# Optimization experiments

Hardware: AMD Instinct MI355X
Metric: run time of the kernel (lower is better)

Reference implementation:

```python
import jax, jax.numpy as jnp
import numpy as np
from jax.scipy.special import logsumexp

SINKHORN_ALPHA = 20.0
OT_MAX_ITER = 100
STOP_THR = 0.005


def setup_inputs() -> dict:
    key = jax.random.key(0)
    k1, k2 = jax.random.split(key)
    x = jax.random.normal(k1, (256, 384), dtype=jnp.float32)   # topic embeddings [K, D]
    y = jax.random.normal(k2, (32768, 384), dtype=jnp.float32)  # word embeddings  [V, D]
    return {"x": x, "y": y}


def reference(x, y):
    n, m = x.shape[0], y.shape[0]
    # FASTopic pairwise_euclidean_distance: squared euclidean cost [n, m]
    M = jnp.sum(x * x, axis=1, keepdims=True) + jnp.sum(y * y, axis=1) - 2.0 * (x @ y.T)
    a = jnp.full((n, 1), 1.0 / n, dtype=M.dtype)
    b = jnp.full((m, 1), 1.0 / m, dtype=M.dtype)
    log_a = jnp.log(a + 1e-30)
    log_b = jnp.log(b + 1e-30)
    log_K0 = -M * SINKHORN_ALPHA

    # State trick: the original mutates log_K only at the periodic absorption step
    # (log_K += log_u + log_v.T). We keep log_K = log_K0 + cum_u + cum_v.T so the
    # carried state is only O(n + m) vectors; math is identical.
    def body(state):
        log_u, log_v, cum_u, cum_v, err, cpt = state
        log_K = log_K0 + cum_u + cum_v.T                                    # [n, m]
        log_v_n = log_b - logsumexp(log_K.T + log_u.T, axis=1)[:, None]     # [m, 1]
        log_u_n = log_a - logsumexp(log_K + log_v_n.T, axis=1)[:, None]     # [n, 1]
        cpt_n = cpt + 1

        def absorb(_):
            cu = cum_u + log_u_n
            cv = cum_v + log_v_n
            lK = log_K0 + cu + cv.T
            # marginal check with log_u = log_v = 0 (matches check_convergence)
            row = jnp.exp(logsumexp(lK, axis=1))[:, None]
            col = jnp.exp(logsumexp(lK, axis=0))[:, None]
            e = jnp.maximum(jnp.max(jnp.abs(row - a)), jnp.max(jnp.abs(col - b)))
            return jnp.zeros_like(log_u_n), jnp.zeros_like(log_v_n), cu, cv, e

        def keep(_):
            return log_u_n, log_v_n, cum_u, cum_v, err

        lu, lv, cu, cv, e = jax.lax.cond(cpt_n % 50 == 1, absorb, keep, None)
        return (lu, lv, cu, cv, e, cpt_n)

    def cond_fn(state):
        err, cpt = state[4], state[5]
        return (err > STOP_THR) & (cpt < OT_MAX_ITER)

    init = (jnp.zeros((n, 1), M.dtype), jnp.zeros((m, 1), M.dtype),
            jnp.zeros((n, 1), M.dtype), jnp.zeros((m, 1), M.dtype),
            jnp.array(1.0, M.dtype), jnp.array(0, jnp.int32))
    log_u, log_v, cum_u, cum_v, _, _ = jax.lax.while_loop(cond_fn, body, init)

    log_K = log_K0 + cum_u + cum_v.T
    transp = jnp.exp(log_u) * (jnp.exp(log_K) * jnp.exp(log_v).T)  # diag(u) K diag(v)
    loss_ETP = jnp.sum(transp * M)
    return loss_ETP, transp
```

## Files before the change

kernel.cpp:

```cpp
#include <hip/hip_runtime.h>
#include <math.h>


#define N_TOPIC 256
#define N_WORD  32768

static constexpr float LOG_A = -5.545177444479562f;
static constexpr float LOG_B = -10.397207708399179f;
static constexpr float BVAL  = 3.0517578125e-05f;

typedef float f32x4 __attribute__((ext_vector_type(4)));
typedef short bf16x8 __attribute__((ext_vector_type(8)));

#define PIN4(v) asm volatile("" : "+v"((v).x), "+v"((v).y), "+v"((v).z), "+v"((v).w))

__global__ __launch_bounds__(256) void init_k(
    const float* __restrict__ x, const float* __restrict__ y,
    float* __restrict__ nx, float* __restrict__ ny, float* __restrict__ su,
    unsigned* __restrict__ colerr, int* __restrict__ active,
    int* __restrict__ counters, float* __restrict__ out)
{
    const int b = blockIdx.x, t = threadIdx.x;
    const int w = t >> 6, l = t & 63;
    if (b < 8192) {
        const int r = (b << 2) + w;
        const float4* y4 = (const float4*)y;
        float4 v = y4[r * 96 + l];
        float s = v.x * v.x + v.y * v.y + v.z * v.z + v.w * v.w;
        if (l < 32) {
            float4 u = y4[r * 96 + 64 + l];
            s += u.x * u.x + u.y * u.y + u.z * u.z + u.w * u.w;
        }
        for (int off = 32; off; off >>= 1) s += __shfl_down(s, off);
        if (l == 0) ny[r] = s;
    } else if (b < 8256) {
        const int r = ((b - 8192) << 2) + w;
        const float4* x4 = (const float4*)x;
        float4 v = x4[r * 96 + l];
        float s = v.x * v.x + v.y * v.y + v.z * v.z + v.w * v.w;
        if (l < 32) {
            float4 u = x4[r * 96 + 64 + l];
            s += u.x * u.x + u.y * u.y + u.z * u.z + u.w * u.w;
        }
        for (int off = 32; off; off >>= 1) s += __shfl_down(s, off);
        if (l == 0) { nx[r] = s; su[r] = -20.f * s; }
    } else {
        for (int k = t; k < 4096; k += 256) counters[k] = 0;
        if (t == 0) { colerr[0] = 0u; colerr[1] = 0u; active[0] = 1; out[0] = 0.f; }
    }
}

static __device__ __forceinline__ void split3(float v, ushort& h0, ushort& h1, ushort& h2)
{
    unsigned u0 = __float_as_uint(v);
    h0 = (ushort)(u0 >> 16);
    float r1 = v - __uint_as_float(u0 & 0xFFFF0000u);
    unsigned u1 = __float_as_uint(r1);
    h1 = (ushort)(u1 >> 16);
    float r2 = r1 - __uint_as_float(u1 & 0xFFFF0000u);
    h2 = (ushort)(__float_as_uint(r2) >> 16);
}

static __device__ __forceinline__ bool bar_arrive(int* cnt, int ph, int t, int* lastf)
{
    __threadfence();
    if (t == 0) *lastf = (atomicAdd(&cnt[ph], 1) == 255);
    __syncthreads();
    return *lastf != 0;
}
static __device__ __forceinline__ void bar_release(int* gen, int ph, int t)
{
    __threadfence();
    if (t == 0) atomicExch(gen, ph);
}
static __device__ __forceinline__ void bar_wait(int* gen, int ph, int t)
{
    if (t == 0) {
        while (atomicCAS(gen, -1, -1) < ph) __builtin_amdgcn_s_sleep(2);
    }
    __syncthreads();
    __threadfence();
}

__global__ __launch_bounds__(256, 1) void fused_k(
    const float* __restrict__ x, const float* __restrict__ y,
    float* __restrict__ G,
    float* __restrict__ su, const float* __restrict__ nx,
    const float* __restrict__ ny, float2* __restrict__ pms,
    float* __restrict__ prow, int* __restrict__ cnt, int* __restrict__ gen,
    unsigned* __restrict__ colerr, int* __restrict__ active,
    float* __restrict__ out)
{
    __shared__ __align__(16) char smem[63488];
    __shared__ int lastf;
    float4* xs4 = (float4*)smem;
    ushort* ys0 = (ushort*)(smem + 32768);
    ushort* ys1 = (ushort*)(smem + 43008);
    ushort* ys2 = (ushort*)(smem + 53248);
    float* su_lds = (float*)smem;
    float* mm    = (float*)(smem + 1024);
    float* ss    = (float*)(smem + 5120);
    float* Mcol  = (float*)(smem + 9216);
    float* Wlds  = (float*)(smem + 9728);
    float* ecol  = (float*)(smem + 10240);
    float* Rlds  = (float*)(smem + 10752);
    float* errb  = (float*)(smem + 11776);
    float* nxl   = (float*)(smem + 12288);
    float* nyl   = (float*)(smem + 13312);
    float* pq    = (float*)(smem + 13824);

    const int t   = threadIdx.x;
    const int b   = blockIdx.x;
    const int w   = t >> 6, ln = t & 63, q = ln >> 4, l15 = ln & 15;
    const int jq  = t & 31, ig = t >> 5;
    const int c0  = jq << 2;
    const int jy0 = b << 7;
    int ph = 1;

    const float4* x4 = (const float4*)x;
    const float4* y4 = (const float4*)y;

    {
        f32x4 acc[4][8];
#pragma unroll
        for (int mi = 0; mi < 4; ++mi)
#pragma unroll
            for (int nj = 0; nj < 8; ++nj) acc[mi][nj] = (f32x4){0.f, 0.f, 0.f, 0.f};

        for (int kc = 0; kc < 12; ++kc) {
            __syncthreads();
#pragma unroll
            for (int p = 0; p < 8; ++p) {
                const int f = (p << 8) + t;
                const int r = f >> 3, c4 = f & 7;
                xs4[(r << 3) + (c4 ^ (r & 7))] = x4[r * 96 + (kc << 3) + c4];
            }
#pragma unroll
            for (int p = 0; p < 4; ++p) {
                const int f = (p << 8) + t;
                const int r = f >> 3, c4 = f & 7;
                float4 vy = y4[(size_t)(jy0 + r) * 96 + (kc << 3) + c4];
                ushort a0,a1,a2,b0,b1,b2,g0,g1,g2,d0,d1,d2;
                split3(vy.x, a0,a1,a2); split3(vy.y, b0,b1,b2);
                split3(vy.z, g0,g1,g2); split3(vy.w, d0,d1,d2);
                *(ushort4*)&ys0[r * 40 + (c4 << 2)] = make_ushort4(a0,b0,g0,d0);
                *(ushort4*)&ys1[r * 40 + (c4 << 2)] = make_ushort4(a1,b1,g1,d1);
                *(ushort4*)&ys2[r * 40 + (c4 << 2)] = make_ushort4(a2,b2,g2,d2);
            }
            __syncthreads();

            union U8 { ushort u[8]; bf16x8 v; };
            bf16x8 A0[4], A1[4], A2[4];
#pragma unroll
            for (int mi = 0; mi < 4; ++mi) {
                const int row = (w << 6) + (mi << 4) + l15;
                const int base = row << 3;
                float4 xa = xs4[base + (((q << 1) + 0) ^ (row & 7))];
                float4 xb = xs4[base + (((q << 1) + 1) ^ (row & 7))];
                U8 u0, u1, u2;
                split3(xa.x, u0.u[0], u1.u[0], u2.u[0]);
                split3(xa.y, u0.u[1], u1.u[1], u2.u[1]);
                split3(xa.z, u0.u[2], u1.u[2], u2.u[2]);
                split3(xa.w, u0.u[3], u1.u[3], u2.u[3]);
                split3(xb.x, u0.u[4], u1.u[4], u2.u[4]);
                split3(xb.y, u0.u[5], u1.u[5], u2.u[5]);
                split3(xb.z, u0.u[6], u1.u[6], u2.u[6]);
                split3(xb.w, u0.u[7], u1.u[7], u2.u[7]);
                A0[mi] = u0.v; A1[mi] = u1.v; A2[mi] = u2.v;
            }
#pragma unroll
            for (int nj = 0; nj < 8; ++nj) {
                const int off = ((nj << 4) + l15) * 40 + (q << 3);
                bf16x8 B0 = *(const bf16x8*)&ys0[off];
                bf16x8 B1 = *(const bf16x8*)&ys1[off];
                bf16x8 B2 = *(const bf16x8*)&ys2[off];
#pragma unroll
                for (int mi = 0; mi < 4; ++mi) {
                    f32x4 c = acc[mi][nj];
                    c = __builtin_amdgcn_mfma_f32_16x16x32_bf16(A0[mi], B0, c, 0, 0, 0);
                    c = __builtin_amdgcn_mfma_f32_16x16x32_bf16(A0[mi], B1, c, 0, 0, 0);
                    c = __builtin_amdgcn_mfma_f32_16x16x32_bf16(A1[mi], B0, c, 0, 0, 0);
                    c = __builtin_amdgcn_mfma_f32_16x16x32_bf16(A1[mi], B1, c, 0, 0, 0);
                    c = __builtin_amdgcn_mfma_f32_16x16x32_bf16(A0[mi], B2, c, 0, 0, 0);
                    c = __builtin_amdgcn_mfma_f32_16x16x32_bf16(A2[mi], B0, c, 0, 0, 0);
                    acc[mi][nj] = c;
                }
            }
        }

#pragma unroll
        for (int mi = 0; mi < 4; ++mi) {
#pragma unroll
            for (int r = 0; r < 4; ++r) {
                const int R = (w << 6) + (mi << 4) + (q << 2) + r;
                float* grow = G + ((size_t)b << 15) + (size_t)R * 128;
#pragma unroll
                for (int nj = 0; nj < 8; ++nj)
                    grow[(nj << 4) + l15] = 40.f * acc[mi][nj][r];
            }
        }
    }

    __syncthreads();

    const float4* G4 = (const float4*)G;
    float4 tile[32];
#pragma unroll
    for (int k = 0; k < 32; ++k) {
        const int i = ig + (k << 3);
        tile[k] = G4[((size_t)b << 13) + (i << 5) + jq];
    }
#pragma unroll
    for (int k = 0; k < 32; ++k) PIN4(tile[k]);

    su_lds[t] = su[t];
    __syncthreads();

    {
        float m0=-INFINITY,m1=-INFINITY,m2=-INFINITY,m3=-INFINITY;
#pragma unroll
        for (int k = 0; k < 32; ++k) {
            const float sk = su_lds[ig + (k << 3)];
            m0=fmaxf(m0,tile[k].x+sk); m1=fmaxf(m1,tile[k].y+sk);
            m2=fmaxf(m2,tile[k].z+sk); m3=fmaxf(m3,tile[k].w+sk);
        }
        float s0=0.f,s1=0.f,s2=0.f,s3=0.f;
#pragma unroll
        for (int k = 0; k < 32; ++k) {
            const float sk = su_lds[ig + (k << 3)];
            s0+=__expf(tile[k].x+sk-m0); s1+=__expf(tile[k].y+sk-m1);
            s2+=__expf(tile[k].z+sk-m2); s3+=__expf(tile[k].w+sk-m3);
        }
        mm[ig*128+c0+0]=m0; ss[ig*128+c0+0]=s0;
        mm[ig*128+c0+1]=m1; ss[ig*128+c0+1]=s1;
        mm[ig*128+c0+2]=m2; ss[ig*128+c0+2]=s2;
        mm[ig*128+c0+3]=m3; ss[ig*128+c0+3]=s3;
        __syncthreads();
        if (t < 128) {
            float m=-INFINITY, s=0.f;
#pragma unroll
            for (int g = 0; g < 8; ++g) {
                float pmv=mm[g*128+t], psv=ss[g*128+t];
                float nm=fmaxf(m,pmv);
                s = s*__expf(m-nm) + psv*__expf(pmv-nm);
                m = nm;
            }
            Wlds[t] = LOG_B - (m + __logf(s));
        }
        __syncthreads();
    }
    {
#pragma unroll
        for (int k = 0; k < 32; ++k) {
            const int i = ig + (k << 3);
            float a0=tile[k].x+Wlds[c0], a1=tile[k].y+Wlds[c0+1];
            float a2=tile[k].z+Wlds[c0+2], a3=tile[k].w+Wlds[c0+3];
            pq[i*33+jq] = fmaxf(fmaxf(a0,a1), fmaxf(a2,a3));
        }
        __syncthreads();
        {
            float R=-INFINITY;
#pragma unroll
            for (int qq = 0; qq < 32; ++qq) R = fmaxf(R, pq[t*33+qq]);
            Rlds[t] = R;
        }
        __syncthreads();
#pragma unroll
        for (int k = 0; k < 32; ++k) {
            const int i = ig + (k << 3);
            const float Rr = Rlds[i];
            float s = __expf(tile[k].x+Wlds[c0]-Rr)   + __expf(tile[k].y+Wlds[c0+1]-Rr)
                    + __expf(tile[k].z+Wlds[c0+2]-Rr) + __expf(tile[k].w+Wlds[c0+3]-Rr);
            pq[i*33+jq] = s;
        }
        __syncthreads();
        {
            float s = 0.f;
#pragma unroll
            for (int qq = 0; qq < 32; ++qq) s += pq[t*33+qq];
            pms[(b << 8) + t] = make_float2(Rlds[t], s);
        }
    }
    if (bar_arrive(cnt, ph, t, &lastf)) {
        __threadfence();
        float m=-INFINITY, s=0.f;
        for (int p = 0; p < 256; ++p) {
            float2 v = pms[(p << 8) + t];
            float nm = fmaxf(m, v.x);
            s = s*__expf(m-nm) + v.y*__expf(v.x-nm);
            m = nm;
        }
        su[t] = LOG_A - (m + __logf(s));
        bar_release(gen, ph, t);
    }
    bar_wait(gen, ph, t); ++ph;
    su_lds[t] = su[t];
    __syncthreads();

    int act;
    {
        float m0=-INFINITY,m1=-INFINITY,m2=-INFINITY,m3=-INFINITY;
#pragma unroll
        for (int k = 0; k < 32; ++k) {
            const float sk = su_lds[ig + (k << 3)];
            m0=fmaxf(m0,tile[k].x+sk); m1=fmaxf(m1,tile[k].y+sk);
            m2=fmaxf(m2,tile[k].z+sk); m3=fmaxf(m3,tile[k].w+sk);
        }
        float s0=0.f,s1=0.f,s2=0.f,s3=0.f;
#pragma unroll
        for (int k = 0; k < 32; ++k) {
            const float sk = su_lds[ig + (k << 3)];
            s0+=__expf(tile[k].x+sk-m0); s1+=__expf(tile[k].y+sk-m1);
            s2+=__expf(tile[k].z+sk-m2); s3+=__expf(tile[k].w+sk-m3);
        }
        mm[ig*128+c0+0]=m0; ss[ig*128+c0+0]=s0;
        mm[ig*128+c0+1]=m1; ss[ig*128+c0+1]=s1;
        mm[ig*128+c0+2]=m2; ss[ig*128+c0+2]=s2;
        mm[ig*128+c0+3]=m3; ss[ig*128+c0+3]=s3;
        __syncthreads();
        if (t < 128) {
            float m=-INFINITY, s=0.f;
#pragma unroll
            for (int g = 0; g < 8; ++g) {
                float pmv=mm[g*128+t], psv=ss[g*128+t];
                float nm=fmaxf(m,pmv);
                s = s*__expf(m-nm) + psv*__expf(pmv-nm);
                m = nm;
            }
            errb[t] = fabsf(__expf((m + __logf(s)) + Wlds[t]) - BVAL);
        }
        __syncthreads();
        for (int n = 64; n; n >>= 1) {
            if (t < n) errb[t] = fmaxf(errb[t], errb[t + n]);
            __syncthreads();
        }
        if (t == 0) atomicMax(&colerr[0], __float_as_uint(errb[0]));
        if (bar_arrive(cnt, ph, t, &lastf)) {
            if (t == 0) {
                unsigned e = atomicMax(&colerr[0], 0u);
                active[0] = (__uint_as_float(e) > 0.005f) ? 1 : 0;
            }
            bar_release(gen, ph, t);
        }
        bar_wait(gen, ph, t); ++ph;
        act = active[0];
    }

    if (act) {
#pragma unroll 1
        for (int tt = 2; tt <= 100; ++tt) {
            {
                float m0=-INFINITY,m1=-INFINITY,m2=-INFINITY,m3=-INFINITY;
#pragma unroll
                for (int k = 0; k < 32; ++k) {
                    const float sk = su_lds[ig + (k << 3)];
                    m0=fmaxf(m0,tile[k].x+sk); m1=fmaxf(m1,tile[k].y+sk);
                    m2=fmaxf(m2,tile[k].z+sk); m3=fmaxf(m3,tile[k].w+sk);
                }
                mm[ig*128+c0+0]=m0; mm[ig*128+c0+1]=m1;
                mm[ig*128+c0+2]=m2; mm[ig*128+c0+3]=m3;
                __syncthreads();
                if (t < 128) {
                    float m=-INFINITY;
#pragma unroll
                    for (int g = 0; g < 8; ++g) m = fmaxf(m, mm[g*128+t]);
                    Mcol[t] = m;
                }
                __syncthreads();
            }
            float4 E[32];
            {
                const float Mc0=Mcol[c0], Mc1=Mcol[c0+1], Mc2=Mcol[c0+2], Mc3=Mcol[c0+3];
                float s0=0.f,s1=0.f,s2=0.f,s3=0.f;
#pragma unroll
                for (int k = 0; k < 32; ++k) {
                    const float sk = su_lds[ig + (k << 3)];
                    E[k].x=__expf(tile[k].x+sk-Mc0); s0+=E[k].x;
                    E[k].y=__expf(tile[k].y+sk-Mc1); s1+=E[k].y;
                    E[k].z=__expf(tile[k].z+sk-Mc2); s2+=E[k].z;
                    E[k].w=__expf(tile[k].w+sk-Mc3); s3+=E[k].w;
                }
                ss[ig*128+c0+0]=s0; ss[ig*128+c0+1]=s1;
                ss[ig*128+c0+2]=s2; ss[ig*128+c0+3]=s3;
                __syncthreads();
                if (t < 128) {
                    float ssum = 0.f;
#pragma unroll
                    for (int g = 0; g < 8; ++g) ssum += ss[g*128+t];
                    Wlds[t] = LOG_B - (Mcol[t] + __logf(ssum));
                    ecol[t] = 1.0f / ssum;
                }
                __syncthreads();
            }
            {
                const float e0=ecol[c0], e1=ecol[c0+1], e2=ecol[c0+2], e3=ecol[c0+3];
#pragma unroll
                for (int k = 0; k < 32; ++k) {
                    const int i = ig + (k << 3);
                    pq[i*33+jq] = E[k].x*e0 + E[k].y*e1 + E[k].z*e2 + E[k].w*e3;
                }
                __syncthreads();
                float s = 0.f;
#pragma unroll
                for (int qq = 0; qq < 32; ++qq) s += pq[t*33+qq];
                prow[(b << 8) + t] = s;
            }
            if (bar_arrive(cnt, ph, t, &lastf)) {
                __threadfence();
                float tot = 0.f;
                for (int p = 0; p < 256; ++p) tot += prow[(p << 8) + t];
                su[t] = (LOG_A - LOG_B) + su_lds[t] - __logf(tot);
                bar_release(gen, ph, t);
            }
            bar_wait(gen, ph, t); ++ph;
            su_lds[t] = su[t];
            __syncthreads();

            if (tt == 51) {
                float m0=-INFINITY,m1=-INFINITY,m2=-INFINITY,m3=-INFINITY;
#pragma unroll
                for (int k = 0; k < 32; ++k) {
                    const float sk = su_lds[ig + (k << 3)];
                    m0=fmaxf(m0,tile[k].x+sk); m1=fmaxf(m1,tile[k].y+sk);
                    m2=fmaxf(m2,tile[k].z+sk); m3=fmaxf(m3,tile[k].w+sk);
                }
                float s0=0.f,s1=0.f,s2=0.f,s3=0.f;
#pragma unroll
                for (int k = 0; k < 32; ++k) {
                    const float sk = su_lds[ig + (k << 3)];
                    s0+=__expf(tile[k].x+sk-m0); s1+=__expf(tile[k].y+sk-m1);
                    s2+=__expf(tile[k].z+sk-m2); s3+=__expf(tile[k].w+sk-m3);
                }
                mm[ig*128+c0+0]=m0; ss[ig*128+c0+0]=s0;
                mm[ig*128+c0+1]=m1; ss[ig*128+c0+1]=s1;
                mm[ig*128+c0+2]=m2; ss[ig*128+c0+2]=s2;
                mm[ig*128+c0+3]=m3; ss[ig*128+c0+3]=s3;
                __syncthreads();
                if (t < 128) {
                    float m=-INFINITY, s=0.f;
#pragma unroll
                    for (int g = 0; g < 8; ++g) {
                        float pmv=mm[g*128+t], psv=ss[g*128+t];
                        float nm=fmaxf(m,pmv);
                        s = s*__expf(m-nm) + psv*__expf(pmv-nm);
                        m = nm;
                    }
                    errb[t] = fabsf(__expf((m + __logf(s)) + Wlds[t]) - BVAL);
                }
                __syncthreads();
                for (int n = 64; n; n >>= 1) {
                    if (t < n) errb[t] = fmaxf(errb[t], errb[t + n]);
                    __syncthreads();
                }
                if (t == 0) atomicMax(&colerr[1], __float_as_uint(errb[0]));
                if (bar_arrive(cnt, ph, t, &lastf)) {
                    if (t == 0) {
                        unsigned e = atomicMax(&colerr[1], 0u);
                        active[0] = (__uint_as_float(e) > 0.005f) ? 1 : 0;
                    }
                    bar_release(gen, ph, t);
                }
                bar_wait(gen, ph, t); ++ph;
                if (active[0] == 0) break;
            }
        }
    }

    nxl[t] = nx[t];
    if (t < 128) nyl[t] = ny[jy0 + t];
    __syncthreads();

    const float Wc0 = Wlds[c0+0], Wc1 = Wlds[c0+1], Wc2 = Wlds[c0+2], Wc3 = Wlds[c0+3];
    const float ny0 = nyl[c0+0], ny1 = nyl[c0+1], ny2 = nyl[c0+2], ny3 = nyl[c0+3];
    float accl = 0.f;
#pragma unroll 4
    for (int k = 0; k < 32; ++k) {
        const int i = ig + (k << 3);
        const float si = su_lds[i], nxi = nxl[i];
        const float g0 = tile[k].x, g1 = tile[k].y, g2 = tile[k].z, g3 = tile[k].w;
        float v0 = __expf(g0 + si + Wc0);
        float v1 = __expf(g1 + si + Wc1);
        float v2 = __expf(g2 + si + Wc2);
        float v3 = __expf(g3 + si + Wc3);
        float* o = out + 1 + (size_t)i * 32768 + jy0 + c0;
        __builtin_nontemporal_store(v0, o + 0);
        __builtin_nontemporal_store(v1, o + 1);
        __builtin_nontemporal_store(v2, o + 2);
        __builtin_nontemporal_store(v3, o + 3);
        accl += v0 * (nxi + ny0 - 0.05f * g0) +
                v1 * (nxi + ny1 - 0.05f * g1) +
                v2 * (nxi + ny2 - 0.05f * g2) +
                v3 * (nxi + ny3 - 0.05f * g3);
    }
    for (int off = 32; off; off >>= 1) accl += __shfl_down(accl, off);
    if (ln == 0) errb[w] = accl;
    __syncthreads();
    if (t == 0) atomicAdd(out, errb[0] + errb[1] + errb[2] + errb[3]);
}

extern "C" void kernel_launch(void* const* d_in, const int* in_sizes, int n_in,
                              void* d_out, int out_size, void* d_ws, size_t ws_size,
                              hipStream_t stream)
{
    const float* x = (const float*)d_in[0];
    const float* y = (const float*)d_in[1];
    float* out = (float*)d_out;

    float* ws   = (float*)d_ws;
    float* G    = ws;
    float* su   = G + 8388608;
    float* nx   = su + 256;
    float* ny   = nx + 256;
    float2* pms = (float2*)(ny + 32768);
    float* prow = (float*)(pms + 65536);
    unsigned* colerr = (unsigned*)(prow + 65536);
    int* active   = (int*)(colerr + 2);
    int* counters = active + 1;
    int* gen      = counters + 3000;

    init_k<<<8257, 256, 0, stream>>>(x, y, nx, ny, su, colerr, active, counters, out);
    fused_k<<<256, 256, 0, stream>>>(x, y, G, su, nx, ny, pms, prow,
                                     counters, gen, colerr, active, out);
}
```

Baseline: 348.0 us.

## Split GEMM into four column passes and stage results into register tile via LDS

The 256x128 distance GEMM per block is split into four 32-column passes with a smaller accumulator (4x2 fragments). Each pass's results go through an LDS exchange buffer straight into the persistent register tile, instead of a global write followed by a global re-read. The tile's column mapping changes from contiguous (c0..c0+3) to strided (jq, jq+32, jq+64, jq+96), and all reductions are updated to match. The epilogue now re-reads G from global memory, since the register tile layout no longer matches the contiguous output layout. This lowers accumulator register pressure and the G round-trip before the Sinkhorn loop, at the cost of reloading x four times and adding more barriers.

```diff
diff --git a/kernel.cpp b/kernel.cpp
--- a/kernel.cpp
+++ b/kernel.cpp
@@ -84,19 +84,20 @@
 
 __global__ __launch_bounds__(256, 1) void fused_k(
     const float* __restrict__ x, const float* __restrict__ y,
-    float* __restrict__ G,
-    float* __restrict__ su, const float* __restrict__ nx,
-    const float* __restrict__ ny, float2* __restrict__ pms,
-    float* __restrict__ prow, int* __restrict__ cnt, int* __restrict__ gen,
+    float* __restrict__ G, float* __restrict__ su,
+    const float* __restrict__ nx, const float* __restrict__ ny,
+    float2* __restrict__ pms, float* __restrict__ prow,
+    int* __restrict__ cnt, int* __restrict__ gen,
     unsigned* __restrict__ colerr, int* __restrict__ active,
     float* __restrict__ out)
 {
-    __shared__ __align__(16) char smem[63488];
+    __shared__ __align__(16) char smem[56832];
     __shared__ int lastf;
     float4* xs4 = (float4*)smem;
     ushort* ys0 = (ushort*)(smem + 32768);
-    ushort* ys1 = (ushort*)(smem + 43008);
-    ushort* ys2 = (ushort*)(smem + 53248);
+    ushort* ys1 = (ushort*)(smem + 35328);
+    ushort* ys2 = (ushort*)(smem + 37888);
+    float*  exb = (float*)(smem + 47616);
     float* su_lds = (float*)smem;
     float* mm    = (float*)(smem + 1024);
     float* ss    = (float*)(smem + 5120);
@@ -109,110 +110,116 @@
     float* nyl   = (float*)(smem + 13312);
     float* pq    = (float*)(smem + 13824);
 
-    const int t   = threadIdx.x;
-    const int b   = blockIdx.x;
-    const int w   = t >> 6, ln = t & 63, q = ln >> 4, l15 = ln & 15;
-    const int jq  = t & 31, ig = t >> 5;
-    const int c0  = jq << 2;
+    const int t  = threadIdx.x;
+    const int b  = blockIdx.x;
+    const int w  = t >> 6, ln = t & 63, q = ln >> 4, l15 = ln & 15;
+    const int jq = t & 31, ig = t >> 5;
+    const int c0 = jq << 2;
     const int jy0 = b << 7;
     int ph = 1;
 
     const float4* x4 = (const float4*)x;
     const float4* y4 = (const float4*)y;
+    const float4* G4 = (const float4*)G;
 
     {
-        f32x4 acc[4][8];
-#pragma unroll
-        for (int mi = 0; mi < 4; ++mi)
-#pragma unroll
-            for (int nj = 0; nj < 8; ++nj) acc[mi][nj] = (f32x4){0.f, 0.f, 0.f, 0.f};
-
-        for (int kc = 0; kc < 12; ++kc) {
-            __syncthreads();
-#pragma unroll
-            for (int p = 0; p < 8; ++p) {
-                const int f = (p << 8) + t;
-                const int r = f >> 3, c4 = f & 7;
-                xs4[(r << 3) + (c4 ^ (r & 7))] = x4[r * 96 + (kc << 3) + c4];
-            }
-#pragma unroll
-            for (int p = 0; p < 4; ++p) {
-                const int f = (p << 8) + t;
-                const int r = f >> 3, c4 = f & 7;
-                float4 vy = y4[(size_t)(jy0 + r) * 96 + (kc << 3) + c4];
-                ushort a0,a1,a2,b0,b1,b2,g0,g1,g2,d0,d1,d2;
-                split3(vy.x, a0,a1,a2); split3(vy.y, b0,b1,b2);
-                split3(vy.z, g0,g1,g2); split3(vy.w, d0,d1,d2);
-                *(ushort4*)&ys0[r * 40 + (c4 << 2)] = make_ushort4(a0,b0,g0,d0);
-                *(ushort4*)&ys1[r * 40 + (c4 << 2)] = make_ushort4(a1,b1,g1,d1);
-                *(ushort4*)&ys2[r * 40 + (c4 << 2)] = make_ushort4(a2,b2,g2,d2);
-            }
-            __syncthreads();
-
-            union U8 { ushort u[8]; bf16x8 v; };
-            bf16x8 A0[4], A1[4], A2[4];
-#pragma unroll
-            for (int mi = 0; mi < 4; ++mi) {
-                const int row = (w << 6) + (mi << 4) + l15;
-                const int base = row << 3;
-                float4 xa = xs4[base + (((q << 1) + 0) ^ (row & 7))];
-                float4 xb = xs4[base + (((q << 1) + 1) ^ (row & 7))];
-                U8 u0, u1, u2;
-                split3(xa.x, u0.u[0], u1.u[0], u2.u[0]);
-                split3(xa.y, u0.u[1], u1.u[1], u2.u[1]);
-                split3(xa.z, u0.u[2], u1.u[2], u2.u[2]);
-                split3(xa.w, u0.u[3], u1.u[3], u2.u[3]);
-                split3(xb.x, u0.u[4], u1.u[4], u2.u[4]);
-                split3(xb.y, u0.u[5], u1.u[5], u2.u[5]);
-                split3(xb.z, u0.u[6], u1.u[6], u2.u[6]);
-                split3(xb.w, u0.u[7], u1.u[7], u2.u[7]);
-                A0[mi] = u0.v; A1[mi] = u1.v; A2[mi] = u2.v;
-            }
-#pragma unroll
-            for (int nj = 0; nj < 8; ++nj) {
-                const int off = ((nj << 4) + l15) * 40 + (q << 3);
-                bf16x8 B0 = *(const bf16x8*)&ys0[off];
-                bf16x8 B1 = *(const bf16x8*)&ys1[off];
-                bf16x8 B2 = *(const bf16x8*)&ys2[off];
-#pragma unroll
-                for (int mi = 0; mi < 4; ++mi) {
-                    f32x4 c = acc[mi][nj];
-                    c = __builtin_amdgcn_mfma_f32_16x16x32_bf16(A0[mi], B0, c, 0, 0, 0);
-                    c = __builtin_amdgcn_mfma_f32_16x16x32_bf16(A0[mi], B1, c, 0, 0, 0);
-                    c = __builtin_amdgcn_mfma_f32_16x16x32_bf16(A1[mi], B0, c, 0, 0, 0);
-                    c = __builtin_amdgcn_mfma_f32_16x16x32_bf16(A1[mi], B1, c, 0, 0, 0);
-                    c = __builtin_amdgcn_mfma_f32_16x16x32_bf16(A0[mi], B2, c, 0, 0, 0);
-                    c = __builtin_amdgcn_mfma_f32_16x16x32_bf16(A2[mi], B0, c, 0, 0, 0);
-                    acc[mi][nj] = c;
-                }
-            }
-        }
-
-#pragma unroll
-        for (int mi = 0; mi < 4; ++mi) {
-#pragma unroll
-            for (int r = 0; r < 4; ++r) {
-                const int R = (w << 6) + (mi << 4) + (q << 2) + r;
-                float* grow = G + ((size_t)b << 15) + (size_t)R * 128;
-#pragma unroll
-                for (int nj = 0; nj < 8; ++nj)
-                    grow[(nj << 4) + l15] = 40.f * acc[mi][nj][r];
-            }
-        }
-    }
-
-    __syncthreads();
-
-    const float4* G4 = (const float4*)G;
     float4 tile[32];
-#pragma unroll
-    for (int k = 0; k < 32; ++k) {
-        const int i = ig + (k << 3);
-        tile[k] = G4[((size_t)b << 13) + (i << 5) + jq];
-    }
+
+#define DO_PASS(PP, CMP)                                                      \
+    {                                                                         \
+        f32x4 acc[4][2];                                                      \
+        _Pragma("unroll")                                                     \
+        for (int mi = 0; mi < 4; ++mi)                                        \
+            _Pragma("unroll")                                                 \
+            for (int nj = 0; nj < 2; ++nj)                                    \
+                acc[mi][nj] = (f32x4){0.f, 0.f, 0.f, 0.f};                    \
+        for (int kc = 0; kc < 12; ++kc) {                                     \
+            __syncthreads();                                                  \
+            _Pragma("unroll")                                                 \
+            for (int p8 = 0; p8 < 8; ++p8) {                                  \
+                const int f = (p8 << 8) + t, r = f >> 3, c4 = f & 7;          \
+                xs4[(r << 3) + (c4 ^ (r & 7))] = x4[r * 96 + (kc << 3) + c4]; \
+            }                                                                 \
+            {                                                                 \
+                const int r = t >> 3, c4 = t & 7;                             \
+                float4 vy = y4[(size_t)(jy0 + (PP << 5) + r) * 96             \
+                               + (kc << 3) + c4];                             \
+                ushort a0,a1,a2,b0,b1,b2,g0,g1,g2,d0,d1,d2;                   \
+                split3(vy.x, a0,a1,a2); split3(vy.y, b0,b1,b2);               \
+                split3(vy.z, g0,g1,g2); split3(vy.w, d0,d1,d2);               \
+                *(ushort4*)&ys0[r*40+(c4<<2)] = make_ushort4(a0,b0,g0,d0);    \
+                *(ushort4*)&ys1[r*40+(c4<<2)] = make_ushort4(a1,b1,g1,d1);    \
+                *(ushort4*)&ys2[r*40+(c4<<2)] = make_ushort4(a2,b2,g2,d2);    \
+            }                                                                 \
+            __syncthreads();                                                  \
+            union U8 { ushort u[8]; bf16x8 v; };                              \
+            _Pragma("unroll")                                                 \
+            for (int mi = 0; mi < 4; ++mi) {                                  \
+                const int row = (w << 6) + (mi << 4) + l15, base = row << 3;  \
+                float4 xa = xs4[base + (((q << 1)    ) ^ (row & 7))];         \
+                float4 xb = xs4[base + (((q << 1) + 1) ^ (row & 7))];         \
+                U8 u0, u1, u2;                                                \
+                split3(xa.x, u0.u[0], u1.u[0], u2.u[0]);                      \
+                split3(xa.y, u0.u[1], u1.u[1], u2.u[1]);                      \
+                split3(xa.z, u0.u[2], u1.u[2], u2.u[2]);                      \
+                split3(xa.w, u0.u[3], u1.u[3], u2.u[3]);                      \
+                split3(xb.x, u0.u[4], u1.u[4], u2.u[4]);                      \
+                split3(xb.y, u0.u[5], u1.u[5], u2.u[5]);                      \
+                split3(xb.z, u0.u[6], u1.u[6], u2.u[6]);                      \
+                split3(xb.w, u0.u[7], u1.u[7], u2.u[7]);                      \
+                _Pragma("unroll")                                             \
+                for (int nj = 0; nj < 2; ++nj) {                              \
+                    const int off = ((nj << 4) + l15) * 40 + (q << 3);        \
+                    bf16x8 B0 = *(const bf16x8*)&ys0[off];                    \
+                    bf16x8 B1 = *(const bf16x8*)&ys1[off];                    \
+                    bf16x8 B2 = *(const bf16x8*)&ys2[off];                    \
+                    f32x4 c = acc[mi][nj];                                    \
+                    c = __builtin_amdgcn_mfma_f32_16x16x32_bf16(u0.v, B0, c, 0, 0, 0); \
+                    c = __builtin_amdgcn_mfma_f32_16x16x32_bf16(u0.v, B1, c, 0, 0, 0); \
+                    c = __builtin_amdgcn_mfma_f32_16x16x32_bf16(u1.v, B0, c, 0, 0, 0); \
+                    c = __builtin_amdgcn_mfma_f32_16x16x32_bf16(u1.v, B1, c, 0, 0, 0); \
+                    c = __builtin_amdgcn_mfma_f32_16x16x32_bf16(u0.v, B2, c, 0, 0, 0); \
+                    c = __builtin_amdgcn_mfma_f32_16x16x32_bf16(u2.v, B0, c, 0, 0, 0); \
+                    acc[mi][nj] = c;                                          \
+                }                                                             \
+            }                                                                 \
+        }                                                                     \
+        _Pragma("unroll")                                                     \
+        for (int c4 = 0; c4 < 4; ++c4) {                                      \
+            __syncthreads();                                                  \
+            if (w == c4) {                                                    \
+                _Pragma("unroll")                                             \
+                for (int mi = 0; mi < 4; ++mi)                                \
+                    _Pragma("unroll")                                         \
+                    for (int nj = 0; nj < 2; ++nj)                            \
+                        _Pragma("unroll")                                     \
+                        for (int r = 0; r < 4; ++r)                           \
+                            exb[((mi << 4) + (q << 2) + r) * 36               \
+                                + (nj << 4) + l15] = 40.f * acc[mi][nj][r];   \
+            }                                                                 \
+            __syncthreads();                                                  \
+            _Pragma("unroll")                                                 \
+            for (int kk = 0; kk < 8; ++kk)                                    \
+                tile[(c4 << 3) + kk].CMP = exb[(ig + (kk << 3)) * 36 + jq];   \
+            _Pragma("unroll")                                                 \
+            for (int cc = 0; cc < 8; ++cc) {                                  \
+                const int idx = (cc << 8) + t, rr = idx >> 5, c31 = idx & 31; \
+                G[(size_t)b * 32768 + (size_t)((c4 << 6) + rr) * 128          \
+                  + (PP << 5) + c31] = exb[rr * 36 + c31];                    \
+            }                                                                 \
+        }                                                                     \
+    }
+
+    DO_PASS(0, x)
+    DO_PASS(1, y)
+    DO_PASS(2, z)
+    DO_PASS(3, w)
+#undef DO_PASS
+
 #pragma unroll
     for (int k = 0; k < 32; ++k) PIN4(tile[k]);
 
+    __syncthreads();
     su_lds[t] = su[t];
     __syncthreads();
 
@@ -231,10 +238,10 @@
             s0+=__expf(tile[k].x+sk-m0); s1+=__expf(tile[k].y+sk-m1);
             s2+=__expf(tile[k].z+sk-m2); s3+=__expf(tile[k].w+sk-m3);
         }
-        mm[ig*128+c0+0]=m0; ss[ig*128+c0+0]=s0;
-        mm[ig*128+c0+1]=m1; ss[ig*128+c0+1]=s1;
-        mm[ig*128+c0+2]=m2; ss[ig*128+c0+2]=s2;
-        mm[ig*128+c0+3]=m3; ss[ig*128+c0+3]=s3;
+        mm[ig*128+jq+ 0]=m0; ss[ig*128+jq+ 0]=s0;
+        mm[ig*128+jq+32]=m1; ss[ig*128+jq+32]=s1;
+        mm[ig*128+jq+64]=m2; ss[ig*128+jq+64]=s2;
+        mm[ig*128+jq+96]=m3; ss[ig*128+jq+96]=s3;
         __syncthreads();
         if (t < 128) {
             float m=-INFINITY, s=0.f;
@@ -250,11 +257,12 @@
         __syncthreads();
     }
     {
+        const float Wc0=Wlds[jq], Wc1=Wlds[jq+32], Wc2=Wlds[jq+64], Wc3=Wlds[jq+96];
 #pragma unroll
         for (int k = 0; k < 32; ++k) {
             const int i = ig + (k << 3);
-            float a0=tile[k].x+Wlds[c0], a1=tile[k].y+Wlds[c0+1];
-            float a2=tile[k].z+Wlds[c0+2], a3=tile[k].w+Wlds[c0+3];
+            float a0=tile[k].x+Wc0, a1=tile[k].y+Wc1;
+            float a2=tile[k].z+Wc2, a3=tile[k].w+Wc3;
             pq[i*33+jq] = fmaxf(fmaxf(a0,a1), fmaxf(a2,a3));
         }
         __syncthreads();
@@ -269,8 +277,8 @@
         for (int k = 0; k < 32; ++k) {
             const int i = ig + (k << 3);
             const float Rr = Rlds[i];
-            float s = __expf(tile[k].x+Wlds[c0]-Rr)   + __expf(tile[k].y+Wlds[c0+1]-Rr)
-                    + __expf(tile[k].z+Wlds[c0+2]-Rr) + __expf(tile[k].w+Wlds[c0+3]-Rr);
+            float s = __expf(tile[k].x+Wc0-Rr) + __expf(tile[k].y+Wc1-Rr)
+                    + __expf(tile[k].z+Wc2-Rr) + __expf(tile[k].w+Wc3-Rr);
             pq[i*33+jq] = s;
         }
         __syncthreads();
@@ -313,10 +321,10 @@
             s0+=__expf(tile[k].x+sk-m0); s1+=__expf(tile[k].y+sk-m1);
             s2+=__expf(tile[k].z+sk-m2); s3+=__expf(tile[k].w+sk-m3);
         }
-        mm[ig*128+c0+0]=m0; ss[ig*128+c0+0]=s0;
-        mm[ig*128+c0+1]=m1; ss[ig*128+c0+1]=s1;
-        mm[ig*128+c0+2]=m2; ss[ig*128+c0+2]=s2;
-        mm[ig*128+c0+3]=m3; ss[ig*128+c0+3]=s3;
+        mm[ig*128+jq+ 0]=m0; ss[ig*128+jq+ 0]=s0;
+        mm[ig*128+jq+32]=m1; ss[ig*128+jq+32]=s1;
+        mm[ig*128+jq+64]=m2; ss[ig*128+jq+64]=s2;
+        mm[ig*128+jq+96]=m3; ss[ig*128+jq+96]=s3;
         __syncthreads();
         if (t < 128) {
             float m=-INFINITY, s=0.f;
@@ -357,8 +365,8 @@
                     m0=fmaxf(m0,tile[k].x+sk); m1=fmaxf(m1,tile[k].y+sk);
                     m2=fmaxf(m2,tile[k].z+sk); m3=fmaxf(m3,tile[k].w+sk);
                 }
-                mm[ig*128+c0+0]=m0; mm[ig*128+c0+1]=m1;
-                mm[ig*128+c0+2]=m2; mm[ig*128+c0+3]=m3;
+                mm[ig*128+jq+ 0]=m0; mm[ig*128+jq+32]=m1;
+                mm[ig*128+jq+64]=m2; mm[ig*128+jq+96]=m3;
                 __syncthreads();
                 if (t < 128) {
                     float m=-INFINITY;
@@ -370,7 +378,7 @@
             }
             float4 E[32];
             {
-                const float Mc0=Mcol[c0], Mc1=Mcol[c0+1], Mc2=Mcol[c0+2], Mc3=Mcol[c0+3];
+                const float Mc0=Mcol[jq], Mc1=Mcol[jq+32], Mc2=Mcol[jq+64], Mc3=Mcol[jq+96];
                 float s0=0.f,s1=0.f,s2=0.f,s3=0.f;
 #pragma unroll
                 for (int k = 0; k < 32; ++k) {
@@ -380,8 +388,8 @@
                     E[k].z=__expf(tile[k].z+sk-Mc2); s2+=E[k].z;
                     E[k].w=__expf(tile[k].w+sk-Mc3); s3+=E[k].w;
                 }
-                ss[ig*128+c0+0]=s0; ss[ig*128+c0+1]=s1;
-                ss[ig*128+c0+2]=s2; ss[ig*128+c0+3]=s3;
+                ss[ig*128+jq+ 0]=s0; ss[ig*128+jq+32]=s1;
+                ss[ig*128+jq+64]=s2; ss[ig*128+jq+96]=s3;
                 __syncthreads();
                 if (t < 128) {
                     float ssum = 0.f;
@@ -393,7 +401,7 @@
                 __syncthreads();
             }
             {
-                const float e0=ecol[c0], e1=ecol[c0+1], e2=ecol[c0+2], e3=ecol[c0+3];
+                const float e0=ecol[jq], e1=ecol[jq+32], e2=ecol[jq+64], e3=ecol[jq+96];
 #pragma unroll
                 for (int k = 0; k < 32; ++k) {
                     const int i = ig + (k << 3);
@@ -431,10 +439,10 @@
                     s0+=__expf(tile[k].x+sk-m0); s1+=__expf(tile[k].y+sk-m1);
                     s2+=__expf(tile[k].z+sk-m2); s3+=__expf(tile[k].w+sk-m3);
                 }
-                mm[ig*128+c0+0]=m0; ss[ig*128+c0+0]=s0;
-                mm[ig*128+c0+1]=m1; ss[ig*128+c0+1]=s1;
-                mm[ig*128+c0+2]=m2; ss[ig*128+c0+2]=s2;
-                mm[ig*128+c0+3]=m3; ss[ig*128+c0+3]=s3;
+                mm[ig*128+jq+ 0]=m0; ss[ig*128+jq+ 0]=s0;
+                mm[ig*128+jq+32]=m1; ss[ig*128+jq+32]=s1;
+                mm[ig*128+jq+64]=m2; ss[ig*128+jq+64]=s2;
+                mm[ig*128+jq+96]=m3; ss[ig*128+jq+96]=s3;
                 __syncthreads();
                 if (t < 128) {
                     float m=-INFINITY, s=0.f;
@@ -465,6 +473,7 @@
             }
         }
     }
+    }
 
     nxl[t] = nx[t];
     if (t < 128) nyl[t] = ny[jy0 + t];
@@ -476,21 +485,21 @@
 #pragma unroll 4
     for (int k = 0; k < 32; ++k) {
         const int i = ig + (k << 3);
+        float4 g = G4[((size_t)b << 13) + (i << 5) + jq];
         const float si = su_lds[i], nxi = nxl[i];
-        const float g0 = tile[k].x, g1 = tile[k].y, g2 = tile[k].z, g3 = tile[k].w;
-        float v0 = __expf(g0 + si + Wc0);
-        float v1 = __expf(g1 + si + Wc1);
-        float v2 = __expf(g2 + si + Wc2);
-        float v3 = __expf(g3 + si + Wc3);
+        float v0 = __expf(g.x + si + Wc0);
+        float v1 = __expf(g.y + si + Wc1);
+        float v2 = __expf(g.z + si + Wc2);
+        float v3 = __expf(g.w + si + Wc3);
         float* o = out + 1 + (size_t)i * 32768 + jy0 + c0;
         __builtin_nontemporal_store(v0, o + 0);
         __builtin_nontemporal_store(v1, o + 1);
         __builtin_nontemporal_store(v2, o + 2);
         __builtin_nontemporal_store(v3, o + 3);
-        accl += v0 * (nxi + ny0 - 0.05f * g0) +
-                v1 * (nxi + ny1 - 0.05f * g1) +
-                v2 * (nxi + ny2 - 0.05f * g2) +
-                v3 * (nxi + ny3 - 0.05f * g3);
+        accl += v0 * (nxi + ny0 - 0.05f * g.x) +
+                v1 * (nxi + ny1 - 0.05f * g.y) +
+                v2 * (nxi + ny2 - 0.05f * g.z) +
+                v3 * (nxi + ny3 - 0.05f * g.w);
     }
     for (int off = 32; off; off >>= 1) accl += __shfl_down(accl, off);
     if (ln == 0) errb[w] = accl;
```

Result: slower. 365.2 us (+4.9%).
